# Kernel tuning notes

Hardware: AMD Instinct MI355X
Metric: run time of the kernel (lower is better)

The kernel has to match this reference:

```python
import jax, jax.numpy as jnp
import numpy as np

B, S, D = 8, 4096, 1024
H = 16
HD = D // H          # 64
FF = 128             # FeedForward default intermediate_size
EPS = 1e-6           # flax RMSNorm default


def _rmsnorm(x, g):
    return x * jax.lax.rsqrt(jnp.mean(x * x, axis=-1, keepdims=True) + EPS) * g


def setup_inputs() -> dict:
    key = jax.random.key(0)
    ks = jax.random.split(key, 12)
    s = 0.02
    return {
        "x": jax.random.normal(ks[0], (B, S, D), jnp.float32),
        "attention_mask": jnp.ones((B, HD), jnp.int32),
        # per-head QKV projections stacked over heads: [H, D, HD]
        "Wq": jax.random.normal(ks[1], (H, D, HD), jnp.float32) * s,
        "bq": jnp.zeros((H, HD), jnp.float32),
        "Wk": jax.random.normal(ks[2], (H, D, HD), jnp.float32) * s,
        "bk": jnp.zeros((H, HD), jnp.float32),
        "Wv": jax.random.normal(ks[3], (H, D, HD), jnp.float32) * s,
        "bv": jnp.zeros((H, HD), jnp.float32),
        "Wo": jax.random.normal(ks[4], (D, D), jnp.float32) * s,
        "bo": jnp.zeros((D,), jnp.float32),
        "W1": jax.random.normal(ks[5], (D, FF), jnp.float32) * s,
        "b1": jnp.zeros((FF,), jnp.float32),
        "W2": jax.random.normal(ks[6], (FF, D), jnp.float32) * s,
        "b2": jnp.zeros((D,), jnp.float32),
        "g1": jnp.ones((D,), jnp.float32),
        "g2": jnp.ones((D,), jnp.float32),
    }


def reference(x, attention_mask, Wq, bq, Wk, bk, Wv, bv, Wo, bo, W1, b1, W2, b2, g1, g2):
    # per-head projections, vectorized over heads: [B, H, S, HD]
    q = jnp.einsum('bsd,hde->bhse', x, Wq) + bq[:, None, :]
    k = jnp.einsum('bsd,hde->bhse', x, Wk) + bk[:, None, :]
    v = jnp.einsum('bsd,hde->bhse', x, Wv) + bv[:, None, :]
    # scores = k^T @ q -> [B, H, HD(kfeat), HD(qfeat)]  (feature-feature attention)
    scores = jnp.einsum('bhsk,bhsq->bhkq', k, q)
    # tiled mask: each row of [HD, HD] equals mask -> masks along last (q-feature) axis
    m = attention_mask[:, None, None, :]  # [B,1,1,HD]
    scores = jnp.where(m == 0, -jnp.inf, scores)
    w = jax.nn.softmax(scores / jnp.sqrt(jnp.float32(HD)), axis=-2)
    # out = v @ w -> [B, H, S, HD]
    attn = jnp.einsum('bhsk,bhkq->bhsq', v, w)
    attn = attn.transpose(0, 2, 1, 3).reshape(B, S, D)  # concat heads
    # output projection + residual + RMSNorm
    h = x + attn @ Wo + bo
    h = _rmsnorm(h, g1)
    # tanh FFN + residual + RMSNorm
    ff = jnp.tanh(h @ W1 + b1) @ W2 + b2
    out = _rmsnorm(h + ff, g2)
    return out
```

## Files before the change

### kernel.cpp

```cpp
#include <hip/hip_runtime.h>
#include <math.h>

typedef __attribute__((ext_vector_type(4))) float f32x4;
typedef __attribute__((ext_vector_type(8))) short short8;
typedef __attribute__((ext_vector_type(4))) short short4v;

__device__ __forceinline__ float b2f(unsigned short u) {
  unsigned int x = ((unsigned int)u) << 16;
  return __builtin_bit_cast(float, x);
}
__device__ __forceinline__ unsigned short f2b(float f) {
  unsigned int x = __builtin_bit_cast(unsigned int, f);
  x += 0x7fffu + ((x >> 16) & 1u);
  return (unsigned short)(x >> 16);
}

__device__ __forceinline__ void gload16(const unsigned short* g, unsigned short* l) {
  __builtin_amdgcn_global_load_lds(
      (__attribute__((address_space(1))) void*)(unsigned long long)(const void*)g,
      (__attribute__((address_space(3))) void*)l, 16, 0, 0);
}

#define BARR  { __builtin_amdgcn_sched_barrier(0); __builtin_amdgcn_s_barrier(); __builtin_amdgcn_sched_barrier(0); }
#define LBARR { __builtin_amdgcn_sched_barrier(0); asm volatile("s_waitcnt lgkmcnt(0)" ::: "memory"); __builtin_amdgcn_s_barrier(); __builtin_amdgcn_sched_barrier(0); }
#define VMW(n) { __builtin_amdgcn_sched_barrier(0); asm volatile("s_waitcnt vmcnt(" #n ")" ::: "memory"); __builtin_amdgcn_sched_barrier(0); }

__global__ __launch_bounds__(256) void prep_kernel(
    const float* __restrict__ x, unsigned short* __restrict__ xb,
    const float* __restrict__ Wq, const float* __restrict__ Wk,
    const float* __restrict__ Wv, const float* __restrict__ Wo,
    const float* __restrict__ W1, const float* __restrict__ W2,
    const float* __restrict__ bq, const float* __restrict__ bk, const float* __restrict__ bv,
    const float* __restrict__ g1,
    unsigned short* __restrict__ BqkvT, unsigned short* __restrict__ WoT,
    unsigned short* __restrict__ W1T, unsigned short* __restrict__ W2T,
    float* __restrict__ bqkv) {
  __shared__ float tile[64][65];
  int nb = blockIdx.x, t = threadIdx.x;
  if (nb < 16384) {
    long i = (long)nb * 256 + t;
    f32x4 a = ((const f32x4*)x)[i * 2];
    f32x4 b = ((const f32x4*)x)[i * 2 + 1];
    short8 o;
#pragma unroll
    for (int j = 0; j < 4; ++j) { o[j] = (short)f2b(a[j]); o[4 + j] = (short)f2b(b[j]); }
    ((short8*)xb)[i] = o;
    return;
  }
  int n0 = nb - 16384;
  if (n0 == 1088) {
#pragma unroll
    for (int it = 0; it < 12; ++it) {
      int idx = it * 256 + t;
      float v = (idx < 1024) ? bq[idx] : (idx < 2048 ? bk[idx - 1024] : bv[idx - 2048]);
      bqkv[idx] = v;
    }
    return;
  }
  const float* src; unsigned short* dst; int sld, dld;
  bool foldg = false; int dbase = 0;
  if (n0 < 768) {
    int w = n0 >> 8, rem = n0 & 255, h = rem >> 4, dc = rem & 15;
    const float* W = (w == 0) ? Wq : (w == 1 ? Wk : Wv);
    src = W + ((long)h * 1024 + dc * 64) * 64;                 sld = 64;
    dst = BqkvT + (long)(w * 1024 + h * 64) * 1024 + dc * 64;  dld = 1024;
  } else if (n0 < 1024) {
    int rem = n0 - 768, dr = rem >> 4, jc = rem & 15;
    src = Wo + (long)dr * 64 * 1024 + jc * 64;                 sld = 1024;
    dst = WoT + (long)jc * 64 * 1024 + dr * 64;                dld = 1024;
  } else if (n0 < 1056) {
    int rem = n0 - 1024, dr = rem >> 1, fc = rem & 1;
    src = W1 + (long)dr * 64 * 128 + fc * 64;                  sld = 128;
    dst = W1T + (long)fc * 64 * 1024 + dr * 64;                dld = 1024;
    foldg = true; dbase = dr * 64;
  } else {
    int rem = n0 - 1056, fr = rem >> 4, jc = rem & 15;
    src = W2 + (long)fr * 64 * 1024 + jc * 64;                 sld = 1024;
    dst = W2T + (long)jc * 64 * 128 + fr * 64;                 dld = 128;
  }
  int r = t >> 2, c0 = (t & 3) * 16;
#pragma unroll
  for (int j4 = 0; j4 < 4; ++j4) {
    f32x4 v = *(const f32x4*)(src + (long)r * sld + c0 + j4 * 4);
    tile[c0 + j4 * 4 + 0][r] = v[0];
    tile[c0 + j4 * 4 + 1][r] = v[1];
    tile[c0 + j4 * 4 + 2][r] = v[2];
    tile[c0 + j4 * 4 + 3][r] = v[3];
  }
  __syncthreads();
  short8 o0, o1;
#pragma unroll
  for (int j = 0; j < 8; ++j) {
    float v0 = tile[r][c0 + j], v1 = tile[r][c0 + 8 + j];
    if (foldg) { v0 *= g1[dbase + c0 + j]; v1 *= g1[dbase + c0 + 8 + j]; }
    o0[j] = (short)f2b(v0);
    o1[j] = (short)f2b(v1);
  }
  *(short8*)(dst + (long)r * dld + c0) = o0;
  *(short8*)(dst + (long)r * dld + c0 + 8) = o1;
}

__device__ __forceinline__ void rdA2(short8 (&dst)[4][2], const char* paK0,
                                     const char* paK1, int off) {
#pragma unroll
  for (int fr = 0; fr < 4; ++fr) {
    dst[fr][0] = *(const short8*)(paK0 + off + fr * 2048);
    dst[fr][1] = *(const short8*)(paK1 + off + fr * 2048);
  }
}
__device__ __forceinline__ void rdB2(short8 (&dst)[2][2], const char* pbK0,
                                     const char* pbK1, int off) {
#pragma unroll
  for (int gr = 0; gr < 2; ++gr) {
    dst[gr][0] = *(const short8*)(pbK0 + off + gr * 2048);
    dst[gr][1] = *(const short8*)(pbK1 + off + gr * 2048);
  }
}
template <int BPH>
__device__ __forceinline__ void mfmaq_f(const short8 (&afr)[4][2], const short8 (&bf)[2][2],
                                        f32x4 (*ac)[4]) {
  __builtin_amdgcn_s_setprio(1);
#pragma unroll
  for (int fi = 0; fi < 4; ++fi)
#pragma unroll
    for (int gj = 0; gj < 2; ++gj)
#pragma unroll
      for (int ks = 0; ks < 2; ++ks)
        ac[fi][BPH * 2 + gj] = __builtin_amdgcn_mfma_f32_16x16x32_bf16(
            afr[fi][ks], bf[gj][ks], ac[fi][BPH * 2 + gj], 0, 0, 0);
  __builtin_amdgcn_s_setprio(0);
}

template <int EPI, int BSEL>
__global__ __launch_bounds__(512, 2) void gemm8p(
    const unsigned short* __restrict__ A, int lda,
    const unsigned short* __restrict__ Bt, int ldb,
    unsigned short* __restrict__ C, int ldc,
    const float* __restrict__ bias,
    const float* __restrict__ residf,
    const unsigned short* __restrict__ residb, int ldr,
    const float* __restrict__ rs, const float* __restrict__ g1f,
    int K, int NBX) {
  extern __shared__ char smb[];
  const int tid = threadIdx.x;
  const int lane = tid & 63, wid = tid >> 6;
  const int wm = wid >> 2, wn = wid & 3;

  int orig = blockIdx.x;
  int xcd = orig & 7, j = orig >> 3;
  int ms = j / (4 * NBX), nb = (j >> 2) % NBX, mq = j & 3;
  const long m0 = (long)(xcd * 16 + ms * 4 + mq) * 256;
  const long n0 = (long)nb * 256;
  const unsigned short* bt = BSEL ? (Bt + (m0 >> 12) * 1048576) : Bt;

  const int NT = K >> 6, NI = NT >> 1;

  const int lr = lane & 15, lc = (lane >> 4) * 16;
  const int eA = lc ^ ((lr & 7) << 4);
  const char* paK0 = smb + wm * 8192 + lr * 128 + eA;
  const char* paK1 = smb + wm * 8192 + lr * 128 + (eA ^ 64);
  const char* pbK0 = smb + 65536 + wn * 4096 + lr * 128 + eA;
  const char* pbK1 = smb + 65536 + wn * 4096 + lr * 128 + (eA ^ 64);

  short8 afr0[4][2], afr1[4][2];
  short8 bfr0[2][2], bfr1[2][2];
  f32x4 acc[8][4] = {};

  auto stA = [&](int buf, int ph, int kt) {
#pragma unroll
    for (int rnd = 0; rnd < 2; ++rnd) {
      int o = rnd * 8192 + tid * 16;
      int wms = o >> 13, rsw = (o >> 7) & 63, cb = o & 127;
      int pcb = cb ^ ((rsw & 7) << 4);
      const unsigned short* src = A + (m0 + wms * 128 + ph * 64 + rsw) * (long)lda + kt * 64 + (pcb >> 1);
      gload16(src, (unsigned short*)(smb + buf * 32768 + ph * 16384 + o));
    }
  };
  auto stB = [&](int buf, int ph, int kt) {
#pragma unroll
    for (int rnd = 0; rnd < 2; ++rnd) {
      int o = rnd * 8192 + tid * 16;
      int wns = (o >> 12) & 3, rsw = (o >> 7) & 31, cb = o & 127;
      int pcb = cb ^ ((rsw & 7) << 4);
      const unsigned short* src = bt + (n0 + wns * 64 + ph * 32 + rsw) * (long)ldb + kt * 64 + (pcb >> 1);
      gload16(src, (unsigned short*)(smb + 65536 + buf * 32768 + ph * 16384 + o));
    }
  };

  stA(0, 0, 0); stA(0, 1, 0); stB(0, 0, 0); stB(0, 1, 0);
  stA(1, 0, 1); stA(1, 1, 1); stB(1, 0, 1); stB(1, 1, 1);
  VMW(8);
  BARR;
  rdA2(afr0, paK0, paK1, 0);
  rdB2(bfr0, pbK0, pbK1, 0);

  for (int i = 0; i < NI; ++i) {
    int t2 = 2 * i + 2, t3 = 2 * i + 3;
    bool more = t2 < NT;
    LBARR;
    rdB2(bfr1, pbK0, pbK1, 16384);
    mfmaq_f<0>(afr0, bfr0, &acc[0]);
    LBARR;
    rdA2(afr1, paK0, paK1, 16384);
    mfmaq_f<1>(afr0, bfr1, &acc[0]);
    LBARR;
    if (more) { stA(0, 0, t2); stA(0, 1, t2); }
    mfmaq_f<0>(afr1, bfr0, &acc[4]);
    if (more) { VMW(4); } else { VMW(0); }
    LBARR;
    rdA2(afr0, paK0, paK1, 32768);
    rdB2(bfr0, pbK0, pbK1, 32768);
    if (more) { stB(0, 0, t2); stB(0, 1, t2); }
    mfmaq_f<1>(afr1, bfr1, &acc[4]);
    LBARR;
    rdB2(bfr1, pbK0, pbK1, 32768 + 16384);
    mfmaq_f<0>(afr0, bfr0, &acc[0]);
    LBARR;
    rdA2(afr1, paK0, paK1, 32768 + 16384);
    mfmaq_f<1>(afr0, bfr1, &acc[0]);
    LBARR;
    if (more) { stA(1, 0, t3); stA(1, 1, t3); }
    mfmaq_f<0>(afr1, bfr0, &acc[4]);
    if (more) { VMW(4); } else { VMW(0); }
    LBARR;
    if (more) { rdA2(afr0, paK0, paK1, 0); rdB2(bfr0, pbK0, pbK1, 0); }
    if (more) { stB(1, 0, t3); stB(1, 1, t3); }
    mfmaq_f<1>(afr1, bfr1, &acc[4]);
  }

#pragma unroll
  for (int f = 0; f < 8; ++f) {
#pragma unroll
    for (int g = 0; g < 4; ++g) {
      long col = n0 + wn * 64 + g * 16 + (lane & 15);
      float bv = bias[col];
      float gv = (EPI == 5) ? g1f[col] : 0.0f;
#pragma unroll
      for (int r = 0; r < 4; ++r) {
        long row = m0 + wm * 128 + f * 16 + (lane >> 4) * 4 + r;
        float o = acc[f][g][r] + bv;
        if (EPI == 1) o += residf[row * (long)ldr + col];
        if (EPI == 3) o += b2f(residb[row * (long)ldr + col]);
        if (EPI == 5) o += b2f(residb[row * (long)ldr + col]) * rs[row] * gv;
        C[row * (long)ldc + col] = f2b(o);
      }
    }
  }
}

template <int EPI>
__global__ __launch_bounds__(256, 2) void gemm_bt(
    const unsigned short* __restrict__ A, int lda,
    const unsigned short* __restrict__ Bt, int ldb,
    unsigned short* __restrict__ C, int ldc,
    const float* __restrict__ bias, const float* __restrict__ rs, int K) {
  __shared__ __align__(16) unsigned short Asm[128 * 32];
  __shared__ __align__(16) unsigned short Bsm[128 * 32];
  const int tid = threadIdx.x;
  const int lane = tid & 63, wid = tid >> 6;
  const int wr = wid >> 1, wc = wid & 1;
  const long m0 = (long)blockIdx.y * 128;
  const long n0 = (long)blockIdx.x * 128;

  f32x4 acc[4][4] = {};

  for (int kk = 0; kk < K; kk += 32) {
    __syncthreads();
#pragma unroll
    for (int i = 0; i < 2; ++i) {
      int slot = i * 256 + tid;
      int r = slot >> 2, cg = (slot & 3) * 8;
      gload16(A + (m0 + r) * (long)lda + kk + cg, &Asm[slot * 8]);
      gload16(Bt + (n0 + r) * (long)ldb + kk + cg, &Bsm[slot * 8]);
    }
    __syncthreads();
    short8 af[4], bfr[4];
#pragma unroll
    for (int mt = 0; mt < 4; ++mt)
      af[mt] = *(const short8*)&Asm[(wr * 64 + mt * 16 + (lane & 15)) * 32 + (lane >> 4) * 8];
#pragma unroll
    for (int nt = 0; nt < 4; ++nt)
      bfr[nt] = *(const short8*)&Bsm[(wc * 64 + nt * 16 + (lane & 15)) * 32 + (lane >> 4) * 8];
#pragma unroll
    for (int mt = 0; mt < 4; ++mt)
#pragma unroll
      for (int nt = 0; nt < 4; ++nt)
        acc[mt][nt] = __builtin_amdgcn_mfma_f32_16x16x32_bf16(af[mt], bfr[nt], acc[mt][nt], 0, 0, 0);
  }

  const long row0 = m0 + wr * 64 + ((lane >> 4) * 4);
  const long col0 = n0 + wc * 64 + (lane & 15);
#pragma unroll
  for (int mt = 0; mt < 4; ++mt) {
#pragma unroll
    for (int nt = 0; nt < 4; ++nt) {
      long col = col0 + nt * 16;
      float bv = bias[col];
      f32x4 v = acc[mt][nt];
#pragma unroll
      for (int r = 0; r < 4; ++r) {
        long row = row0 + mt * 16 + r;
        float o = v[r];
        if (EPI == 4) o = tanhf(o * rs[row] + bv);
        else o += bv;
        C[row * (long)ldc + col] = f2b(o);
      }
    }
  }
}

__device__ __forceinline__ int sperm(int e) { return ((e + (e >> 3)) & 7) << 4; }

__global__ __launch_bounds__(256) void scores_mfma(
    const unsigned short* __restrict__ QKV, float* __restrict__ part) {
  __shared__ __align__(16) char lds[32768];
  int bh = blockIdx.x, seg = blockIdx.y;
  int b = bh >> 4, h = bh & 15;
  int tid = threadIdx.x, lane = tid & 63, wid = tid >> 6;
  int e0 = (tid & 7) * 8;
  int sl0 = (tid >> 3) * 4;
  const unsigned short* Qg = QKV + h * 64;
  const unsigned short* Kg = QKV + 1024 + h * 64;
  f32x4 acc[4] = {};

  for (int ch = 0; ch < 8; ++ch) {
    long S0 = (long)b * 4096 + seg * 1024 + ch * 128;
    __syncthreads();
    short8 kv0 = *(const short8*)(Kg + (S0 + sl0 + 0) * 3072 + e0);
    short8 kv1 = *(const short8*)(Kg + (S0 + sl0 + 1) * 3072 + e0);
    short8 kv2 = *(const short8*)(Kg + (S0 + sl0 + 2) * 3072 + e0);
    short8 kv3 = *(const short8*)(Kg + (S0 + sl0 + 3) * 3072 + e0);
    short8 qv0 = *(const short8*)(Qg + (S0 + sl0 + 0) * 3072 + e0);
    short8 qv1 = *(const short8*)(Qg + (S0 + sl0 + 1) * 3072 + e0);
    short8 qv2 = *(const short8*)(Qg + (S0 + sl0 + 2) * 3072 + e0);
    short8 qv3 = *(const short8*)(Qg + (S0 + sl0 + 3) * 3072 + e0);
#pragma unroll
    for (int je = 0; je < 8; ++je) {
      int e = e0 + je;
      int sw = sperm(e);
      char* rowK = lds + e * 256;
      char* rowQ = lds + 16384 + e * 256;
      unsigned int klo = (unsigned short)kv0[je] | ((unsigned int)(unsigned short)kv1[je] << 16);
      unsigned int khi = (unsigned short)kv2[je] | ((unsigned int)(unsigned short)kv3[je] << 16);
      unsigned int qlo = (unsigned short)qv0[je] | ((unsigned int)(unsigned short)qv1[je] << 16);
      unsigned int qhi = (unsigned short)qv2[je] | ((unsigned int)(unsigned short)qv3[je] << 16);
      *(unsigned int*)(rowK + ((sl0 * 2) ^ sw)) = klo;
      *(unsigned int*)(rowK + ((sl0 * 2 + 4) ^ sw)) = khi;
      *(unsigned int*)(rowQ + ((sl0 * 2) ^ sw)) = qlo;
      *(unsigned int*)(rowQ + ((sl0 * 2 + 4) ^ sw)) = qhi;
    }
    __syncthreads();
#pragma unroll
    for (int ksi = 0; ksi < 4; ++ksi) {
      int colb = ksi * 64 + (lane >> 4) * 16;
      int erA = wid * 16 + (lane & 15);
      short8 af = *(const short8*)(lds + erA * 256 + (colb ^ sperm(erA)));
#pragma unroll
      for (int n = 0; n < 4; ++n) {
        int erB = n * 16 + (lane & 15);
        short8 bf = *(const short8*)(lds + 16384 + erB * 256 + (colb ^ sperm(erB)));
        acc[n] = __builtin_amdgcn_mfma_f32_16x16x32_bf16(af, bf, acc[n], 0, 0, 0);
      }
    }
  }
  float* dst = part + ((long)bh * 4 + seg) * 4096;
#pragma unroll
  for (int n = 0; n < 4; ++n)
#pragma unroll
    for (int r = 0; r < 4; ++r) {
      int k = wid * 16 + (lane >> 4) * 4 + r;
      int q = n * 16 + (lane & 15);
      dst[k * 64 + q] = acc[n][r];
    }
}

__global__ __launch_bounds__(64) void softmax_Wb(
    const float* __restrict__ part, const int* __restrict__ mask,
    unsigned short* __restrict__ Wb) {
  __shared__ float lt[64][65];
  int bh = blockIdx.x, q = threadIdx.x;
  int b = bh >> 4;
  const float* p0 = part + (long)bh * 4 * 4096;
  float s[64];
#pragma unroll
  for (int k = 0; k < 64; ++k)
    s[k] = p0[k * 64 + q] + p0[4096 + k * 64 + q] + p0[8192 + k * 64 + q] + p0[12288 + k * 64 + q];
  bool live = (mask[b * 64 + q] != 0);
  float m = -1e30f;
#pragma unroll
  for (int k = 0; k < 64; ++k) m = fmaxf(m, s[k]);
  float sum = 0.0f;
#pragma unroll
  for (int k = 0; k < 64; ++k) {
    s[k] = __expf((s[k] - m) * 0.125f);
    sum += s[k];
  }
  float inv = live ? 1.0f / sum : 0.0f;
#pragma unroll
  for (int k = 0; k < 64; ++k) lt[k][q] = s[k] * inv;
  __syncthreads();
  unsigned short* o = Wb + (long)bh * 4096 + q * 64;
#pragma unroll
  for (int j8 = 0; j8 < 8; ++j8) {
    short8 ov;
#pragma unroll
    for (int j = 0; j < 8; ++j) ov[j] = (short)f2b(lt[q][j8 * 8 + j]);
    *(short8*)(o + j8 * 8) = ov;
  }
}

__global__ __launch_bounds__(256) void wpt_kernel(
    const unsigned short* __restrict__ WoT, const unsigned short* __restrict__ Wb,
    unsigned short* __restrict__ WPT) {
  int dblk = blockIdx.x;
  int h = blockIdx.y;
  int b = blockIdx.z;
  int tid = threadIdx.x, lane = tid & 63, wid = tid >> 6;
  int d0 = dblk * 256 + wid * 64;
  const unsigned short* wb = Wb + (long)(b * 16 + h) * 4096;
  f32x4 acc[4][4] = {};
#pragma unroll
  for (int ks = 0; ks < 2; ++ks) {
    short8 bf[4];
#pragma unroll
    for (int nt = 0; nt < 4; ++nt)
      bf[nt] = *(const short8*)(wb + (nt * 16 + (lane & 15)) * 64 + ks * 32 + (lane >> 4) * 8);
#pragma unroll
    for (int mt = 0; mt < 4; ++mt) {
      short8 af = *(const short8*)(WoT + (long)(d0 + mt * 16 + (lane & 15)) * 1024 + h * 64 + ks * 32 + (lane >> 4) * 8);
#pragma unroll
      for (int nt = 0; nt < 4; ++nt)
        acc[mt][nt] = __builtin_amdgcn_mfma_f32_16x16x32_bf16(af, bf[nt], acc[mt][nt], 0, 0, 0);
    }
  }
#pragma unroll
  for (int mt = 0; mt < 4; ++mt)
#pragma unroll
    for (int nt = 0; nt < 4; ++nt)
#pragma unroll
      for (int r = 0; r < 4; ++r) {
        long row = d0 + mt * 16 + (lane >> 4) * 4 + r;
        int col = h * 64 + nt * 16 + (lane & 15);
        WPT[(long)b * 1048576 + row * 1024 + col] = f2b(acc[mt][nt][r]);
      }
}

__global__ __launch_bounds__(256) void rowscale_k(
    const unsigned short* __restrict__ in, float* __restrict__ rs) {
  long row = blockIdx.x;
  int tid = threadIdx.x;
  short4v u = *(const short4v*)(in + row * 1024 + tid * 4);
  float ss = 0.0f;
#pragma unroll
  for (int i = 0; i < 4; ++i) {
    float v = b2f((unsigned short)u[i]);
    ss += v * v;
  }
#pragma unroll
  for (int off = 32; off > 0; off >>= 1) ss += __shfl_xor(ss, off, 64);
  __shared__ float wsum[4];
  if ((tid & 63) == 0) wsum[tid >> 6] = ss;
  __syncthreads();
  if (tid == 0) {
    float tot = wsum[0] + wsum[1] + wsum[2] + wsum[3];
    rs[row] = rsqrtf(tot * (1.0f / 1024.0f) + 1e-6f);
  }
}

__global__ __launch_bounds__(256) void rmsnorm_k(
    const unsigned short* __restrict__ in, const float* __restrict__ g,
    float* __restrict__ outf) {
  long row = blockIdx.x;
  int tid = threadIdx.x;
  short4v u = *(const short4v*)(in + row * 1024 + tid * 4);
  float v[4];
  float ss = 0.0f;
#pragma unroll
  for (int i = 0; i < 4; ++i) {
    v[i] = b2f((unsigned short)u[i]);
    ss += v[i] * v[i];
  }
#pragma unroll
  for (int off = 32; off > 0; off >>= 1) ss += __shfl_xor(ss, off, 64);
  __shared__ float wsum[4];
  if ((tid & 63) == 0) wsum[tid >> 6] = ss;
  __syncthreads();
  float tot = wsum[0] + wsum[1] + wsum[2] + wsum[3];
  float rsv = rsqrtf(tot * (1.0f / 1024.0f) + 1e-6f);
  f32x4 gv = *(const f32x4*)(g + tid * 4);
  f32x4 ov;
#pragma unroll
  for (int i = 0; i < 4; ++i) ov[i] = v[i] * rsv * gv[i];
  *(f32x4*)(outf + row * 1024 + tid * 4) = ov;
}

extern "C" void kernel_launch(void* const* d_in, const int* in_sizes, int n_in,
                              void* d_out, int out_size, void* d_ws, size_t ws_size,
                              hipStream_t stream) {
  const float* x  = (const float*)d_in[0];
  const int* mask = (const int*)d_in[1];
  const float* Wq = (const float*)d_in[2];
  const float* bq = (const float*)d_in[3];
  const float* Wk = (const float*)d_in[4];
  const float* bk = (const float*)d_in[5];
  const float* Wv = (const float*)d_in[6];
  const float* bv = (const float*)d_in[7];
  const float* Wo = (const float*)d_in[8];
  const float* bo = (const float*)d_in[9];
  const float* W1 = (const float*)d_in[10];
  const float* b1 = (const float*)d_in[11];
  const float* W2 = (const float*)d_in[12];
  const float* b2 = (const float*)d_in[13];
  const float* g1 = (const float*)d_in[14];
  const float* g2 = (const float*)d_in[15];

  char* ws = (char*)d_ws;
  size_t off = 0;
  auto alc = [&](size_t n) { size_t o = off; off += (n + 255) & ~(size_t)255; return o; };
  unsigned short* BqkvT = (unsigned short*)(ws + alc(3072UL * 1024 * 2));
  unsigned short* WoT   = (unsigned short*)(ws + alc(1024UL * 1024 * 2));
  unsigned short* W1T   = (unsigned short*)(ws + alc(128UL * 1024 * 2));
  unsigned short* W2T   = (unsigned short*)(ws + alc(1024UL * 128 * 2));
  float*          bqkv  = (float*)(ws + alc(3072UL * 4));
  unsigned short* R0    = (unsigned short*)(ws + alc(32768UL * 1024 * 2));
  unsigned short* R1    = (unsigned short*)(ws + alc(32768UL * 3072 * 2));
  unsigned short* R2    = (unsigned short*)(ws + alc(32768UL * 1024 * 2));
  unsigned short* WPb   = (unsigned short*)(ws + alc(8UL * 1024 * 1024 * 2));
  unsigned short* Tb    = (unsigned short*)(ws + alc(32768UL * 128 * 2));
  float*          SP    = (float*)(ws + alc(512UL * 4096 * 4));
  unsigned short* Wbuf  = (unsigned short*)(ws + alc(128UL * 4096 * 2));
  float*          RSb   = (float*)(ws + alc(32768UL * 4));
  if (ws_size < off) return;

  unsigned short* xb   = R0;
  unsigned short* HFb  = R0;
  unsigned short* QKVb = R1;
  unsigned short* H1b  = R2;
  float* outp = (float*)d_out;

  prep_kernel<<<17473, 256, 0, stream>>>(x, xb, Wq, Wk, Wv, Wo, W1, W2, bq, bk, bv, g1,
                                         BqkvT, WoT, W1T, W2T, bqkv);
  gemm8p<0, 0><<<1536, 512, 131072, stream>>>(xb, 1024, BqkvT, 1024, QKVb, 3072,
                                              bqkv, nullptr, nullptr, 0, nullptr, nullptr,
                                              1024, 12);
  scores_mfma<<<dim3(128, 4), 256, 0, stream>>>(QKVb, SP);
  softmax_Wb<<<128, 64, 0, stream>>>(SP, mask, Wbuf);
  wpt_kernel<<<dim3(4, 16, 8), 256, 0, stream>>>(WoT, Wbuf, WPb);
  gemm8p<3, 1><<<512, 512, 131072, stream>>>(QKVb + 2048, 3072, WPb, 1024, H1b, 1024,
                                             bo, nullptr, xb, 1024, nullptr, nullptr,
                                             1024, 4);
  rowscale_k<<<32768, 256, 0, stream>>>(H1b, RSb);
  gemm_bt<4><<<dim3(1, 256), 256, 0, stream>>>(H1b, 1024, W1T, 1024, Tb, 128, b1, RSb, 1024);
  gemm8p<5, 0><<<512, 512, 131072, stream>>>(Tb, 128, W2T, 128, HFb, 1024,
                                             b2, nullptr, H1b, 1024, RSb, g1,
                                             128, 4);
  rmsnorm_k<<<32768, 256, 0, stream>>>(HFb, g2, outp);
}
```

Baseline: 508.7 us.

## Fold V projection into per-batch attention-output weight, drop V GEMM

Instead of computing V = x·Wv over all tokens and then multiplying by a per-batch combined matrix, the code precomputes per-batch W = Wv_rearranged · (softmax-weights ⊗ Wo) with a small GEMM. It then applies that to x directly, with the V bias folded in through a small dot-product kernel into a per-batch output bias. This removes one third of the large QKV projection GEMM and the V intermediate write and read. The cost is an extra small per-batch GEMM and a bias kernel, plus an extra bf16 rounding of the fused weight.

Result: faster. 466.5 us (median of 2 runs) (-8.3%).

```diff
diff --git a/kernel.cpp b/kernel.cpp
--- a/kernel.cpp
+++ b/kernel.cpp
@@ -32,8 +32,9 @@
     const float* __restrict__ W1, const float* __restrict__ W2,
     const float* __restrict__ bq, const float* __restrict__ bk, const float* __restrict__ bv,
     const float* __restrict__ g1,
-    unsigned short* __restrict__ BqkvT, unsigned short* __restrict__ WoT,
+    unsigned short* __restrict__ BqkT, unsigned short* __restrict__ WoT,
     unsigned short* __restrict__ W1T, unsigned short* __restrict__ W2T,
+    unsigned short* __restrict__ WvR,
     float* __restrict__ bqkv) {
   __shared__ float tile[64][65];
   int nb = blockIdx.x, t = threadIdx.x;
@@ -57,24 +58,39 @@
     }
     return;
   }
+  if (n0 >= 832) {
+    int rem = n0 - 832, h = rem >> 4, dc = rem & 15;
+    int r = t >> 2, c0 = (t & 3) * 16;
+    const float* s = Wv + ((long)h * 1024 + dc * 64 + r) * 64 + c0;
+    unsigned short* d = WvR + (long)(dc * 64 + r) * 1024 + h * 64 + c0;
+#pragma unroll
+    for (int j4 = 0; j4 < 4; ++j4) {
+      f32x4 v = *(const f32x4*)(s + j4 * 4);
+      short4v o;
+#pragma unroll
+      for (int j = 0; j < 4; ++j) o[j] = (short)f2b(v[j]);
+      *(short4v*)(d + j4 * 4) = o;
+    }
+    return;
+  }
   const float* src; unsigned short* dst; int sld, dld;
   bool foldg = false; int dbase = 0;
-  if (n0 < 768) {
+  if (n0 < 512) {
     int w = n0 >> 8, rem = n0 & 255, h = rem >> 4, dc = rem & 15;
-    const float* W = (w == 0) ? Wq : (w == 1 ? Wk : Wv);
+    const float* W = (w == 0) ? Wq : Wk;
     src = W + ((long)h * 1024 + dc * 64) * 64;                 sld = 64;
-    dst = BqkvT + (long)(w * 1024 + h * 64) * 1024 + dc * 64;  dld = 1024;
-  } else if (n0 < 1024) {
-    int rem = n0 - 768, dr = rem >> 4, jc = rem & 15;
+    dst = BqkT + (long)(w * 1024 + h * 64) * 1024 + dc * 64;   dld = 1024;
+  } else if (n0 < 768) {
+    int rem = n0 - 512, dr = rem >> 4, jc = rem & 15;
     src = Wo + (long)dr * 64 * 1024 + jc * 64;                 sld = 1024;
     dst = WoT + (long)jc * 64 * 1024 + dr * 64;                dld = 1024;
-  } else if (n0 < 1056) {
-    int rem = n0 - 1024, dr = rem >> 1, fc = rem & 1;
+  } else if (n0 < 800) {
+    int rem = n0 - 768, dr = rem >> 1, fc = rem & 1;
     src = W1 + (long)dr * 64 * 128 + fc * 64;                  sld = 128;
     dst = W1T + (long)fc * 64 * 1024 + dr * 64;                dld = 1024;
     foldg = true; dbase = dr * 64;
   } else {
-    int rem = n0 - 1056, fr = rem >> 4, jc = rem & 15;
+    int rem = n0 - 800, fr = rem >> 4, jc = rem & 15;
     src = W2 + (long)fr * 64 * 1024 + jc * 64;                 sld = 1024;
     dst = W2T + (long)jc * 64 * 128 + fr * 64;                 dld = 128;
   }
@@ -131,13 +147,12 @@
   __builtin_amdgcn_s_setprio(0);
 }
 
-template <int EPI, int BSEL>
+template <int EPI, int BSEL, int BBIAS>
 __global__ __launch_bounds__(512, 2) void gemm8p(
     const unsigned short* __restrict__ A, int lda,
     const unsigned short* __restrict__ Bt, int ldb,
     unsigned short* __restrict__ C, int ldc,
     const float* __restrict__ bias,
-    const float* __restrict__ residf,
     const unsigned short* __restrict__ residb, int ldr,
     const float* __restrict__ rs, const float* __restrict__ g1f,
     int K, int NBX) {
@@ -148,10 +163,13 @@
 
   int orig = blockIdx.x;
   int xcd = orig & 7, j = orig >> 3;
+  int perx = gridDim.x >> 3;
+  int mpx = perx / NBX;
   int ms = j / (4 * NBX), nb = (j >> 2) % NBX, mq = j & 3;
-  const long m0 = (long)(xcd * 16 + ms * 4 + mq) * 256;
+  const long m0 = (long)(xcd * mpx + ms * 4 + mq) * 256;
   const long n0 = (long)nb * 256;
   const unsigned short* bt = BSEL ? (Bt + (m0 >> 12) * 1048576) : Bt;
+  const float* biasp = BBIAS ? (bias + (m0 >> 12) * 1024) : bias;
 
   const int NT = K >> 6, NI = NT >> 1;
 
@@ -233,13 +251,12 @@
 #pragma unroll
     for (int g = 0; g < 4; ++g) {
       long col = n0 + wn * 64 + g * 16 + (lane & 15);
-      float bv = bias[col];
+      float bv = (EPI == 6) ? 0.0f : biasp[col];
       float gv = (EPI == 5) ? g1f[col] : 0.0f;
 #pragma unroll
       for (int r = 0; r < 4; ++r) {
         long row = m0 + wm * 128 + f * 16 + (lane >> 4) * 4 + r;
         float o = acc[f][g][r] + bv;
-        if (EPI == 1) o += residf[row * (long)ldr + col];
         if (EPI == 3) o += b2f(residb[row * (long)ldr + col]);
         if (EPI == 5) o += b2f(residb[row * (long)ldr + col]) * rs[row] * gv;
         C[row * (long)ldc + col] = f2b(o);
@@ -312,28 +329,28 @@
 __device__ __forceinline__ int sperm(int e) { return ((e + (e >> 3)) & 7) << 4; }
 
 __global__ __launch_bounds__(256) void scores_mfma(
-    const unsigned short* __restrict__ QKV, float* __restrict__ part) {
+    const unsigned short* __restrict__ QK, float* __restrict__ part) {
   __shared__ __align__(16) char lds[32768];
   int bh = blockIdx.x, seg = blockIdx.y;
   int b = bh >> 4, h = bh & 15;
   int tid = threadIdx.x, lane = tid & 63, wid = tid >> 6;
   int e0 = (tid & 7) * 8;
   int sl0 = (tid >> 3) * 4;
-  const unsigned short* Qg = QKV + h * 64;
-  const unsigned short* Kg = QKV + 1024 + h * 64;
+  const unsigned short* Qg = QK + h * 64;
+  const unsigned short* Kg = QK + 1024 + h * 64;
   f32x4 acc[4] = {};
 
   for (int ch = 0; ch < 8; ++ch) {
     long S0 = (long)b * 4096 + seg * 1024 + ch * 128;
     __syncthreads();
-    short8 kv0 = *(const short8*)(Kg + (S0 + sl0 + 0) * 3072 + e0);
-    short8 kv1 = *(const short8*)(Kg + (S0 + sl0 + 1) * 3072 + e0);
-    short8 kv2 = *(const short8*)(Kg + (S0 + sl0 + 2) * 3072 + e0);
-    short8 kv3 = *(const short8*)(Kg + (S0 + sl0 + 3) * 3072 + e0);
-    short8 qv0 = *(const short8*)(Qg + (S0 + sl0 + 0) * 3072 + e0);
-    short8 qv1 = *(const short8*)(Qg + (S0 + sl0 + 1) * 3072 + e0);
-    short8 qv2 = *(const short8*)(Qg + (S0 + sl0 + 2) * 3072 + e0);
-    short8 qv3 = *(const short8*)(Qg + (S0 + sl0 + 3) * 3072 + e0);
+    short8 kv0 = *(const short8*)(Kg + (S0 + sl0 + 0) * 2048 + e0);
+    short8 kv1 = *(const short8*)(Kg + (S0 + sl0 + 1) * 2048 + e0);
+    short8 kv2 = *(const short8*)(Kg + (S0 + sl0 + 2) * 2048 + e0);
+    short8 kv3 = *(const short8*)(Kg + (S0 + sl0 + 3) * 2048 + e0);
+    short8 qv0 = *(const short8*)(Qg + (S0 + sl0 + 0) * 2048 + e0);
+    short8 qv1 = *(const short8*)(Qg + (S0 + sl0 + 1) * 2048 + e0);
+    short8 qv2 = *(const short8*)(Qg + (S0 + sl0 + 2) * 2048 + e0);
+    short8 qv3 = *(const short8*)(Qg + (S0 + sl0 + 3) * 2048 + e0);
 #pragma unroll
     for (int je = 0; je < 8; ++je) {
       int e = e0 + je;
@@ -443,6 +460,22 @@
         int col = h * 64 + nt * 16 + (lane & 15);
         WPT[(long)b * 1048576 + row * 1024 + col] = f2b(acc[mt][nt][r]);
       }
+}
+
+__global__ __launch_bounds__(256) void bvdot_kernel(
+    const unsigned short* __restrict__ WPT, const float* __restrict__ bv,
+    const float* __restrict__ bo, float* __restrict__ hb) {
+  int b = blockIdx.y;
+  int dp = blockIdx.x * 256 + threadIdx.x;
+  const unsigned short* row = WPT + (long)b * 1048576 + (long)dp * 1024;
+  float acc = 0.0f;
+#pragma unroll 4
+  for (int c = 0; c < 1024; c += 8) {
+    short8 v = *(const short8*)(row + c);
+#pragma unroll
+    for (int j = 0; j < 8; ++j) acc += b2f((unsigned short)v[j]) * bv[c + j];
+  }
+  hb[b * 1024 + dp] = bo[dp] + acc;
 }
 
 __global__ __launch_bounds__(256) void rowscale_k(
@@ -517,15 +550,18 @@
   char* ws = (char*)d_ws;
   size_t off = 0;
   auto alc = [&](size_t n) { size_t o = off; off += (n + 255) & ~(size_t)255; return o; };
-  unsigned short* BqkvT = (unsigned short*)(ws + alc(3072UL * 1024 * 2));
+  unsigned short* BqkT  = (unsigned short*)(ws + alc(2048UL * 1024 * 2));
   unsigned short* WoT   = (unsigned short*)(ws + alc(1024UL * 1024 * 2));
   unsigned short* W1T   = (unsigned short*)(ws + alc(128UL * 1024 * 2));
   unsigned short* W2T   = (unsigned short*)(ws + alc(1024UL * 128 * 2));
+  unsigned short* WvR   = (unsigned short*)(ws + alc(1024UL * 1024 * 2));
   float*          bqkv  = (float*)(ws + alc(3072UL * 4));
+  float*          HBb   = (float*)(ws + alc(8192UL * 4));
   unsigned short* R0    = (unsigned short*)(ws + alc(32768UL * 1024 * 2));
-  unsigned short* R1    = (unsigned short*)(ws + alc(32768UL * 3072 * 2));
+  unsigned short* R1    = (unsigned short*)(ws + alc(32768UL * 2048 * 2));
   unsigned short* R2    = (unsigned short*)(ws + alc(32768UL * 1024 * 2));
-  unsigned short* WPb   = (unsigned short*)(ws + alc(8UL * 1024 * 1024 * 2));
+  unsigned short* WPb   = (unsigned short*)(ws + alc(8UL * 1048576 * 2));
+  unsigned short* WVPb  = (unsigned short*)(ws + alc(8UL * 1048576 * 2));
   unsigned short* Tb    = (unsigned short*)(ws + alc(32768UL * 128 * 2));
   float*          SP    = (float*)(ws + alc(512UL * 4096 * 4));
   unsigned short* Wbuf  = (unsigned short*)(ws + alc(128UL * 4096 * 2));
@@ -534,25 +570,29 @@
 
   unsigned short* xb   = R0;
   unsigned short* HFb  = R0;
-  unsigned short* QKVb = R1;
+  unsigned short* QKb  = R1;
   unsigned short* H1b  = R2;
   float* outp = (float*)d_out;
 
   prep_kernel<<<17473, 256, 0, stream>>>(x, xb, Wq, Wk, Wv, Wo, W1, W2, bq, bk, bv, g1,
-                                         BqkvT, WoT, W1T, W2T, bqkv);
-  gemm8p<0, 0><<<1536, 512, 131072, stream>>>(xb, 1024, BqkvT, 1024, QKVb, 3072,
-                                              bqkv, nullptr, nullptr, 0, nullptr, nullptr,
-                                              1024, 12);
-  scores_mfma<<<dim3(128, 4), 256, 0, stream>>>(QKVb, SP);
+                                         BqkT, WoT, W1T, W2T, WvR, bqkv);
+  gemm8p<0, 0, 0><<<1024, 512, 131072, stream>>>(xb, 1024, BqkT, 1024, QKb, 2048,
+                                                 bqkv, nullptr, 0, nullptr, nullptr,
+                                                 1024, 8);
+  scores_mfma<<<dim3(128, 4), 256, 0, stream>>>(QKb, SP);
   softmax_Wb<<<128, 64, 0, stream>>>(SP, mask, Wbuf);
   wpt_kernel<<<dim3(4, 16, 8), 256, 0, stream>>>(WoT, Wbuf, WPb);
-  gemm8p<3, 1><<<512, 512, 131072, stream>>>(QKVb + 2048, 3072, WPb, 1024, H1b, 1024,
-                                             bo, nullptr, xb, 1024, nullptr, nullptr,
-                                             1024, 4);
+  gemm8p<6, 0, 0><<<128, 512, 131072, stream>>>(WPb, 1024, WvR, 1024, WVPb, 1024,
+                                                nullptr, nullptr, 0, nullptr, nullptr,
+                                                1024, 4);
+  bvdot_kernel<<<dim3(4, 8), 256, 0, stream>>>(WPb, bqkv + 2048, bo, HBb);
+  gemm8p<3, 1, 1><<<512, 512, 131072, stream>>>(xb, 1024, WVPb, 1024, H1b, 1024,
+                                                HBb, xb, 1024, nullptr, nullptr,
+                                                1024, 4);
   rowscale_k<<<32768, 256, 0, stream>>>(H1b, RSb);
   gemm_bt<4><<<dim3(1, 256), 256, 0, stream>>>(H1b, 1024, W1T, 1024, Tb, 128, b1, RSb, 1024);
-  gemm8p<5, 0><<<512, 512, 131072, stream>>>(Tb, 128, W2T, 128, HFb, 1024,
-                                             b2, nullptr, H1b, 1024, RSb, g1,
-                                             128, 4);
+  gemm8p<5, 0, 0><<<512, 512, 131072, stream>>>(Tb, 128, W2T, 128, HFb, 1024,
+                                                b2, H1b, 1024, RSb, g1,
+                                                128, 4);
   rmsnorm_k<<<32768, 256, 0, stream>>>(HFb, g2, outp);
 }
```
